# Kernel tuning notes

Measured on AMD Instinct MI355X. Metric: run time of the kernel, lower is better.

Reference implementation:

```python
import jax, jax.numpy as jnp
import numpy as np

B, S, D, H = 2, 4096, 512, 8
HD = D // H  # 64


def setup_inputs() -> dict:
    key = jax.random.key(0)
    ks = jax.random.split(key, 9)
    def lin_init(kw, kb, fan_in, fan_out):
        bound = 1.0 / np.sqrt(fan_in)
        W = jax.random.uniform(kw, (fan_in, fan_out), minval=-bound, maxval=bound, dtype=jnp.float32)
        b = jax.random.uniform(kb, (fan_out,), minval=-bound, maxval=bound, dtype=jnp.float32)
        return W, b
    Wq, bq = lin_init(ks[0], ks[1], D, D)
    Wk, bk = lin_init(ks[2], ks[3], D, D)
    Wv, bv = lin_init(ks[4], ks[5], D, D)
    query = jax.random.normal(ks[6], (B, S, D), dtype=jnp.float32)
    key_in = jax.random.normal(ks[7], (B, S, D), dtype=jnp.float32)
    value = jax.random.normal(ks[8], (B, S, D), dtype=jnp.float32)
    return {"query": query, "key": key_in, "value": value,
            "Wq": Wq, "bq": bq, "Wk": Wk, "bk": bk, "Wv": Wv, "bv": bv}


def _split_heads(x):
    # [B, S, D] -> [B, H, S, HD]
    b, s, _ = x.shape
    return x.reshape(b, s, H, HD).transpose(0, 2, 1, 3)


def reference(query, key, value, Wq, bq, Wk, bk, Wv, bv):
    Q = _split_heads(query @ Wq + bq)
    K = _split_heads(key @ Wk + bk)
    V = _split_heads(value @ Wv + bv)
    scale = 1.0 / np.sqrt(HD).astype(np.float32)
    # scores: [B, H, Sq, Sk]
    scores = jnp.einsum('bhqd,bhkd->bhqk', Q, K) * scale
    weights = jax.nn.softmax(scores, axis=-1)
    att = jnp.einsum('bhqk,bhkd->bhqd', weights, V)
    # [B, H, S, HD] -> [B, S, D]
    return att.transpose(0, 2, 1, 3).reshape(query.shape[0], query.shape[1], D)
```

## Files before the change

kernel.cpp:

```cpp
#include <hip/hip_runtime.h>
#include <hip/hip_bf16.h>
#include <cstdint>


typedef __bf16   bf16x8 __attribute__((ext_vector_type(8)));
typedef _Float16 f16x8  __attribute__((ext_vector_type(8)));
typedef float    f32x4  __attribute__((ext_vector_type(4)));
typedef float    f32x16 __attribute__((ext_vector_type(16)));
typedef unsigned int   u32;
typedef unsigned int   u32x4 __attribute__((ext_vector_type(4)));
typedef unsigned short u16;

#define NB  2
#define SEQ 4096
#define DIM 512
#define NH  8
#define HD  64
#define WSZ (DIM * DIM)
#define XSZ (NB * SEQ * DIM)
#define QSZ (NB * NH * SEQ * HD)

__device__ __forceinline__ u16 f2bf(float f) {
    __bf16 h = (__bf16)f; return __builtin_bit_cast(u16, h);
}
__device__ __forceinline__ u16 f2h(float f) {
    _Float16 h = (_Float16)f; return __builtin_bit_cast(u16, h);
}
__device__ __forceinline__ u32 pack_pkrtz(float a, float b) {
    auto pk = __builtin_amdgcn_cvt_pkrtz(a, b);
    return __builtin_bit_cast(u32, pk);
}
__device__ __forceinline__ bf16x8 cvt8p(float4 a, float4 b) {
    bf16x8 o;
    o[0]=(__bf16)a.x; o[1]=(__bf16)a.y; o[2]=(__bf16)a.z; o[3]=(__bf16)a.w;
    o[4]=(__bf16)b.x; o[5]=(__bf16)b.y; o[6]=(__bf16)b.z; o[7]=(__bf16)b.w;
    return o;
}
__device__ __forceinline__ void dma16(const u16* g, u16* l) {
    __builtin_amdgcn_global_load_lds(
        (const __attribute__((address_space(1))) u32*)g,
        (__attribute__((address_space(3))) u32*)l, 16, 0, 0);
}

__global__ __launch_bounds__(256) void xcvt_kernel(
    const float* __restrict__ xq, const float* __restrict__ xk,
    const float* __restrict__ xv, u16* __restrict__ xb)
{
    const int id = blockIdx.x;
    const int p = id >> 10, rest = id & 1023;
    const int mtile = rest >> 4, kk = rest & 15;
    const float* X = (p == 0) ? xq : ((p == 1) ? xk : xv);
    const int t = threadIdx.x;
    const int row = t >> 1, half = t & 1;
    const float* src = X + ((size_t)(mtile * 128 + row)) * DIM + kk * 32 + half * 16;
    u16* dst = xb + (size_t)p * XSZ + ((size_t)(mtile * 16 + kk)) * 4096 + row * 32;
    const int sr = (row ^ (row >> 2)) & 3;
    float4 a0 = ((const float4*)src)[0], a1 = ((const float4*)src)[1];
    float4 a2 = ((const float4*)src)[2], a3 = ((const float4*)src)[3];
    const int c0 = (half * 2) ^ sr, c1 = (half * 2 + 1) ^ sr;
    *(bf16x8*)(dst + (c0 << 3)) = cvt8p(a0, a1);
    *(bf16x8*)(dst + (c1 << 3)) = cvt8p(a2, a3);
}

__global__ __launch_bounds__(256) void wt_kernel(
    const float* __restrict__ Wq, const float* __restrict__ Wk,
    const float* __restrict__ Wv, u16* __restrict__ wtImg)
{
    __shared__ u16 lT[64 * 65];
    const int p = blockIdx.z;
    const float* W = (p == 0) ? Wq : ((p == 1) ? Wk : Wv);
    const int r0 = blockIdx.x * 64, c0 = blockIdx.y * 64;
    const int t = threadIdx.x;
#pragma unroll
    for (int i = 0; i < 16; i++) {
        int idx = i * 256 + t, rowk = idx >> 6, coln = idx & 63;
        lT[coln * 65 + rowk] = f2bf(W[(size_t)(r0 + rowk) * DIM + c0 + coln]);
    }
    __syncthreads();
#pragma unroll
    for (int i = 0; i < 2; i++) {
        const int idx = i * 256 + t;
        const int nl = idx >> 3, ch = idx & 7;
        const int n = c0 + nl;
        const int row = n & 127, ntile = n >> 7;
        const int kk = (r0 >> 5) + (ch >> 2);
        const int sw = (ch & 3) ^ ((row ^ (row >> 2)) & 3);
        u16* d = wtImg + (size_t)p * WSZ + ((size_t)(ntile * 16 + kk)) * 4096
               + row * 32 + (sw << 3);
#pragma unroll
        for (int e = 0; e < 8; e++) d[e] = lT[nl * 65 + ch * 8 + e];
    }
}

__global__ __launch_bounds__(256) void proj_kernel(
    const u16* __restrict__ xb, const u16* __restrict__ wtImg,
    const float* __restrict__ bq, const float* __restrict__ bk,
    const float* __restrict__ bv,
    u16* __restrict__ qb, u16* __restrict__ kbImg, u16* __restrict__ vtImg)
{
    __shared__ u16 smem[16384];

    const int tid = threadIdx.x;
    const int wave = tid >> 6, lane = tid & 63;
    const int l16 = lane & 15, quad = lane >> 4;
    const int wq = wave >> 1, wn = wave & 1;

    const int id = blockIdx.x;
    const int xcd = id & 7, j = id >> 3;
    const int p = j >> 5, t5 = j & 31;
    int mb, nb;
    if (p < 2) { mb = xcd * 8 + (t5 >> 2); nb = t5 & 3; }
    else       { nb = xcd * 8 + (t5 >> 2); mb = t5 & 3; }

    const u16* Abase = (p < 2) ? xb + (size_t)p * XSZ + (size_t)mb * 16 * 4096
                               : wtImg + (size_t)2 * WSZ + (size_t)mb * 16 * 4096;
    const u16* Bbase = (p < 2) ? wtImg + (size_t)p * WSZ + (size_t)nb * 16 * 4096
                               : xb + (size_t)2 * XSZ + (size_t)nb * 16 * 4096;
    const int doff = tid * 8;

    f32x4 acc[4][4];
#pragma unroll
    for (int ms = 0; ms < 4; ms++)
#pragma unroll
        for (int ns = 0; ns < 4; ns++)
#pragma unroll
            for (int jj = 0; jj < 4; jj++) acc[ms][ns][jj] = 0.f;

#pragma unroll
    for (int e = 0; e < 2; e++) {
        dma16(Abase + e * 2048 + doff, smem + e * 2048 + doff);
        dma16(Bbase + e * 2048 + doff, smem + 4096 + e * 2048 + doff);
    }
    Abase += 4096; Bbase += 4096;

    for (int kt = 0; kt < 16; kt++) {
        __syncthreads();
        if (kt < 15) {
            u16* lb = smem + ((kt + 1) & 1) * 8192;
#pragma unroll
            for (int e = 0; e < 2; e++) {
                dma16(Abase + e * 2048 + doff, lb + e * 2048 + doff);
                dma16(Bbase + e * 2048 + doff, lb + 4096 + e * 2048 + doff);
            }
            Abase += 4096; Bbase += 4096;
        }
        const u16* lA = smem + (kt & 1) * 8192;
        const u16* lB = lA + 4096;

        bf16x8 af[4];
#pragma unroll
        for (int ms = 0; ms < 4; ms++) {
            const int row = wq * 64 + ms * 16 + l16;
            const int sr = (row ^ (row >> 2)) & 3;
            af[ms] = *(const bf16x8*)&lA[row * 32 + ((quad ^ sr) << 3)];
        }
#pragma unroll
        for (int ns = 0; ns < 4; ns++) {
            const int rowb = wn * 64 + ns * 16 + l16;
            const int sb = (rowb ^ (rowb >> 2)) & 3;
            const bf16x8 b = *(const bf16x8*)&lB[rowb * 32 + ((quad ^ sb) << 3)];
#pragma unroll
            for (int ms = 0; ms < 4; ms++)
                acc[ms][ns] = __builtin_amdgcn_mfma_f32_16x16x32_bf16(af[ms], b, acc[ms][ns], 0, 0, 0);
        }
    }

    __syncthreads();
    if (p < 2) {
        const float* bias = p ? bk : bq;
        const float cs = (p == 0) ? 0.18033688011112042f : 1.0f;
        const int stl = wn * 2 + wq;
        const int hh = nb * 2 + wn;
#pragma unroll
        for (int ns = 0; ns < 4; ns++) {
            const int ch = ns * 16 + l16;
            const float bval = bias[hh * 64 + ch];
#pragma unroll
            for (int ms = 0; ms < 4; ms++)
#pragma unroll
                for (int rr = 0; rr < 4; rr++) {
                    const int sqL = ms * 16 + quad * 4 + rr;
                    const float v = (acc[ms][ns][rr] + bval) * cs;
                    int off;
                    if (p == 0) off = sqL * 64 + ch;
                    else        off = sqL * 64 +
                                      (((ch >> 3) ^ ((sqL ^ (sqL >> 3)) & 7)) << 3) + (ch & 7);
                    smem[stl * 4096 + off] = f2bf(v);
                }
        }
    } else {
        const int stl = wq * 2 + wn;
#pragma unroll
        for (int ms = 0; ms < 4; ms++)
#pragma unroll
            for (int rr = 0; rr < 4; rr++) {
                const int hd = ms * 16 + quad * 4 + rr;
                const float bval = bv[mb * 128 + wq * 64 + hd];
                const int swh = (hd ^ (hd >> 3)) & 7;
#pragma unroll
                for (int ns = 0; ns < 4; ns++) {
                    const int nl = ns * 16 + l16;
                    const int sqpL = (nl & ~12) | ((nl & 8) >> 1) | ((nl & 4) << 1);
                    smem[stl * 4096 + hd * 64 +
                         (((sqpL >> 3) ^ swh) << 3) + (sqpL & 7)] =
                        f2h(acc[ms][ns][rr] + bval);
                }
            }
    }
    __syncthreads();

    {
        u16* dstp; size_t gbase;
        if (p < 2) {
            const int hh = nb * 2 + (wave >> 1);
            const int b2 = mb >> 5;
            const int row0 = (mb * 128 + (wave & 1) * 64) & 4095;
            if (p == 0) { dstp = qb;    gbase = ((size_t)(b2 * NH + hh) * 4096 + row0) * 64; }
            else        { dstp = kbImg; gbase = ((size_t)((b2 * NH + hh) * 64 + (row0 >> 6))) * 4096; }
        } else {
            const int hh = mb * 2 + (wave >> 1);
            const int b2 = nb >> 5;
            const int nblk = (nb & 31) * 2 + (wave & 1);
            dstp = vtImg; gbase = ((size_t)((b2 * NH + hh) * 64 + nblk)) * 4096;
        }
#pragma unroll
        for (int e = 0; e < 8; e++) {
            const u32x4 vv = *(const u32x4*)&smem[wave * 4096 + e * 512 + lane * 8];
            *(u32x4*)(dstp + gbase + e * 512 + lane * 8) = vv;
        }
    }
}

__global__ __launch_bounds__(512, 4) void attn_kernel(
    const u16* __restrict__ qb, const u16* __restrict__ kbImg,
    const u16* __restrict__ vtImg, float* __restrict__ out)
{
    __shared__ u16 smem[2 * 4 * 4096];
    float* cmb = (float*)smem;

    const int tid = threadIdx.x;
    const int wave = tid >> 6, lane = tid & 63;
    const int m31 = lane & 31, h = lane >> 5;
    const int wq = wave >> 1, kh = wave & 1;

    const int blk = blockIdx.x;
    const int xcd = blk & 7, idx = blk >> 3;
    const int bh = xcd * 2 + (idx >> 5);
    const int qt = idx & 31;
    const int qbase = qt * 128 + wq * 32;

    bf16x8 qF[4];
#pragma unroll
    for (int c = 0; c < 4; c++)
        qF[c] = *(const bf16x8*)(qb + ((size_t)bh * SEQ + qbase + m31) * HD + c * 16 + h * 8);

    f32x16 O0, O1;
#pragma unroll
    for (int j = 0; j < 16; j++) { O0[j] = 0.f; O1[j] = 0.f; }
    float l_acc = 0.f;

    const int st  = wave >> 1;
    const int hw  = wave & 1;
    const u16* img = (st & 1) ? vtImg : kbImg;
    const u16* gp = img + ((size_t)(bh * 64 + (st >> 1) * 32)) * 4096 + hw * 2048 + lane * 8;
    {
        u16* lb = smem + st * 4096 + hw * 2048 + lane * 8;
#pragma unroll
        for (int e = 0; e < 4; e++) dma16(gp + e * 512, lb + e * 512);
        gp += 4096;
    }

    const int NT = 32;
    for (int it = 0; it < NT; it++) {
        __syncthreads();
        if (it + 1 < NT) {
            u16* lb = smem + ((((it + 1) & 1) * 4 + st)) * 4096 + hw * 2048 + lane * 8;
#pragma unroll
            for (int e = 0; e < 4; e++) dma16(gp + e * 512, lb + e * 512);
            gp += 4096;
        }
        const u16* sK = smem + (size_t)(((it & 1) * 4) + kh * 2) * 4096;
        const u16* sV = sK + 4096;

#pragma unroll
        for (int kg = 0; kg < 2; kg++) {
            const int rK = kg * 32 + m31;
            const int swK = (rK ^ (rK >> 3)) & 7;
            bf16x8 kA[4];
#pragma unroll
            for (int c = 0; c < 4; c++)
                kA[c] = *(const bf16x8*)&sK[(rK << 6) + (((2 * c + h) ^ swK) << 3)];

            const int swV0 = (m31 ^ (m31 >> 3)) & 7;
            const int rV1 = 32 + m31;
            const int swV1 = (rV1 ^ (rV1 >> 3)) & 7;
            f16x8 vA0[2], vA1[2];
#pragma unroll
            for (int c2 = 0; c2 < 2; c2++) {
                vA0[c2] = *(const f16x8*)&sV[(m31 << 6) + (((4 * kg + 2 * c2 + h) ^ swV0) << 3)];
                vA1[c2] = *(const f16x8*)&sV[(rV1 << 6) + (((4 * kg + 2 * c2 + h) ^ swV1) << 3)];
            }

            f32x16 Sv;
#pragma unroll
            for (int j = 0; j < 16; j++) Sv[j] = 0.f;
#pragma unroll
            for (int c = 0; c < 4; c++)
                Sv = __builtin_amdgcn_mfma_f32_32x32x16_bf16(kA[c], qF[c], Sv, 0, 0, 0);

            float ps = 0.f;
            u32 P32[8];
#pragma unroll
            for (int mm = 0; mm < 8; mm++) {
                const float e0 = __builtin_amdgcn_exp2f(Sv[2 * mm]);
                const float e1 = __builtin_amdgcn_exp2f(Sv[2 * mm + 1]);
                ps += e0 + e1;
                P32[mm] = pack_pkrtz(e0, e1);
            }
            l_acc += ps;

            u32x4 f0, f1;
            f0[0] = P32[0]; f0[1] = P32[1]; f0[2] = P32[2]; f0[3] = P32[3];
            f1[0] = P32[4]; f1[1] = P32[5]; f1[2] = P32[6]; f1[3] = P32[7];
            const f16x8 pf0 = __builtin_bit_cast(f16x8, f0);
            const f16x8 pf1 = __builtin_bit_cast(f16x8, f1);
            O0 = __builtin_amdgcn_mfma_f32_32x32x16_f16(vA0[0], pf0, O0, 0, 0, 0);
            O0 = __builtin_amdgcn_mfma_f32_32x32x16_f16(vA0[1], pf1, O0, 0, 0, 0);
            O1 = __builtin_amdgcn_mfma_f32_32x32x16_f16(vA1[0], pf0, O1, 0, 0, 0);
            O1 = __builtin_amdgcn_mfma_f32_32x32x16_f16(vA1[1], pf1, O1, 0, 0, 0);
        }
    }

    l_acc += __shfl_xor(l_acc, 32);
    __syncthreads();
    if (kh == 1) {
#pragma unroll
        for (int hg = 0; hg < 2; hg++)
#pragma unroll
            for (int mm = 0; mm < 4; mm++) {
                f32x4 o;
#pragma unroll
                for (int j = 0; j < 4; j++) o[j] = (hg ? O1 : O0)[4 * mm + j];
                *(f32x4*)&cmb[(((wq * 2 + hg) * 4 + mm) << 8) + lane * 4] = o;
            }
        cmb[8192 + wq * 64 + lane] = l_acc;
    }
    __syncthreads();

    if (kh == 0) {
        const int b = bh >> 3, hcol = bh & 7;
        const float lt = l_acc + cmb[8192 + wq * 64 + lane];
        const float inv = 1.0f / lt;
        const int sq = qbase + m31;
#pragma unroll
        for (int hg = 0; hg < 2; hg++)
#pragma unroll
            for (int mm = 0; mm < 4; mm++) {
                const f32x4 po = *(const f32x4*)&cmb[(((wq * 2 + hg) * 4 + mm) << 8) + lane * 4];
                f32x4 o;
#pragma unroll
                for (int j = 0; j < 4; j++)
                    o[j] = ((hg ? O1 : O0)[4 * mm + j] + po[j]) * inv;
                *(f32x4*)&out[(((size_t)(b * SEQ + sq)) << 9) + hcol * 64
                              + hg * 32 + 8 * mm + 4 * h] = o;
            }
    }
}

extern "C" void kernel_launch(void* const* d_in, const int* in_sizes, int n_in,
                              void* d_out, int out_size, void* d_ws, size_t ws_size,
                              hipStream_t stream)
{
    const float* q  = (const float*)d_in[0];
    const float* k  = (const float*)d_in[1];
    const float* v  = (const float*)d_in[2];
    const float* Wq = (const float*)d_in[3];
    const float* bq = (const float*)d_in[4];
    const float* Wk = (const float*)d_in[5];
    const float* bk = (const float*)d_in[6];
    const float* Wv = (const float*)d_in[7];
    const float* bv = (const float*)d_in[8];
    float* out = (float*)d_out;

    u16* xb  = (u16*)d_ws;
    u16* wti = xb  + (size_t)3 * XSZ;
    u16* qbp = wti + (size_t)3 * WSZ;
    u16* kbp = qbp + (size_t)QSZ;
    u16* vtp = kbp + (size_t)QSZ;

    xcvt_kernel<<<dim3(3072),   256, 0, stream>>>(q, k, v, xb);
    wt_kernel  <<<dim3(8, 8, 3), 256, 0, stream>>>(Wq, Wk, Wv, wti);
    proj_kernel<<<dim3(768),    256, 0, stream>>>(xb, wti, bq, bk, bv,
                                                  qbp, kbp, vtp);
    attn_kernel<<<dim3(512),    512, 0, stream>>>(qbp, kbp, vtp, out);
}
```

Before: 216.4 us.

## Fuse input bf16 conversion into projection and read K/V directly from global in attention

Drops the separate fp32-to-bf16 input conversion kernel. The projection kernel now loads fp32 activations into registers, converts them and writes swizzled bf16 into LDS, while weights are stored plainly transposed and DMA'd with the swizzle applied at load time. The attention kernel drops its LDS double-buffered K/V staging and reads K/V fragments straight from global memory (relying on cache), using smaller 256-thread blocks over 64-query tiles with twice as many blocks. This saves a kernel launch and a full intermediate write/read of the activations, but risks uncoalesced or cache-dependent global loads in attention and register pressure in the projection.

```diff
diff --git a/kernel.cpp b/kernel.cpp
--- a/kernel.cpp
+++ b/kernel.cpp
@@ -17,7 +17,6 @@
 #define NH  8
 #define HD  64
 #define WSZ (DIM * DIM)
-#define XSZ (NB * SEQ * DIM)
 #define QSZ (NB * NH * SEQ * HD)
 
 __device__ __forceinline__ u16 f2bf(float f) {
@@ -42,58 +41,32 @@
         (__attribute__((address_space(3))) u32*)l, 16, 0, 0);
 }
 
-__global__ __launch_bounds__(256) void xcvt_kernel(
-    const float* __restrict__ xq, const float* __restrict__ xk,
-    const float* __restrict__ xv, u16* __restrict__ xb)
-{
-    const int id = blockIdx.x;
-    const int p = id >> 10, rest = id & 1023;
-    const int mtile = rest >> 4, kk = rest & 15;
-    const float* X = (p == 0) ? xq : ((p == 1) ? xk : xv);
-    const int t = threadIdx.x;
-    const int row = t >> 1, half = t & 1;
-    const float* src = X + ((size_t)(mtile * 128 + row)) * DIM + kk * 32 + half * 16;
-    u16* dst = xb + (size_t)p * XSZ + ((size_t)(mtile * 16 + kk)) * 4096 + row * 32;
-    const int sr = (row ^ (row >> 2)) & 3;
-    float4 a0 = ((const float4*)src)[0], a1 = ((const float4*)src)[1];
-    float4 a2 = ((const float4*)src)[2], a3 = ((const float4*)src)[3];
-    const int c0 = (half * 2) ^ sr, c1 = (half * 2 + 1) ^ sr;
-    *(bf16x8*)(dst + (c0 << 3)) = cvt8p(a0, a1);
-    *(bf16x8*)(dst + (c1 << 3)) = cvt8p(a2, a3);
-}
-
 __global__ __launch_bounds__(256) void wt_kernel(
     const float* __restrict__ Wq, const float* __restrict__ Wk,
-    const float* __restrict__ Wv, u16* __restrict__ wtImg)
+    const float* __restrict__ Wv, u16* __restrict__ wt)
 {
     __shared__ u16 lT[64 * 65];
     const int p = blockIdx.z;
     const float* W = (p == 0) ? Wq : ((p == 1) ? Wk : Wv);
+    u16* dst = wt + (size_t)p * WSZ;
     const int r0 = blockIdx.x * 64, c0 = blockIdx.y * 64;
     const int t = threadIdx.x;
 #pragma unroll
     for (int i = 0; i < 16; i++) {
-        int idx = i * 256 + t, rowk = idx >> 6, coln = idx & 63;
-        lT[coln * 65 + rowk] = f2bf(W[(size_t)(r0 + rowk) * DIM + c0 + coln]);
+        int idx = i * 256 + t, row = idx >> 6, col = idx & 63;
+        lT[col * 65 + row] = f2bf(W[(size_t)(r0 + row) * DIM + c0 + col]);
     }
     __syncthreads();
 #pragma unroll
-    for (int i = 0; i < 2; i++) {
-        const int idx = i * 256 + t;
-        const int nl = idx >> 3, ch = idx & 7;
-        const int n = c0 + nl;
-        const int row = n & 127, ntile = n >> 7;
-        const int kk = (r0 >> 5) + (ch >> 2);
-        const int sw = (ch & 3) ^ ((row ^ (row >> 2)) & 3);
-        u16* d = wtImg + (size_t)p * WSZ + ((size_t)(ntile * 16 + kk)) * 4096
-               + row * 32 + (sw << 3);
-#pragma unroll
-        for (int e = 0; e < 8; e++) d[e] = lT[nl * 65 + ch * 8 + e];
+    for (int i = 0; i < 16; i++) {
+        int idx = i * 256 + t, n = idx >> 6, k = idx & 63;
+        dst[(size_t)(c0 + n) * DIM + r0 + k] = lT[n * 65 + k];
     }
 }
 
 __global__ __launch_bounds__(256) void proj_kernel(
-    const u16* __restrict__ xb, const u16* __restrict__ wtImg,
+    const float* __restrict__ xq, const float* __restrict__ xk,
+    const float* __restrict__ xv, const u16* __restrict__ wt,
     const float* __restrict__ bq, const float* __restrict__ bk,
     const float* __restrict__ bv,
     u16* __restrict__ qb, u16* __restrict__ kbImg, u16* __restrict__ vtImg)
@@ -112,11 +85,31 @@
     if (p < 2) { mb = xcd * 8 + (t5 >> 2); nb = t5 & 3; }
     else       { nb = xcd * 8 + (t5 >> 2); mb = t5 & 3; }
 
-    const u16* Abase = (p < 2) ? xb + (size_t)p * XSZ + (size_t)mb * 16 * 4096
-                               : wtImg + (size_t)2 * WSZ + (size_t)mb * 16 * 4096;
-    const u16* Bbase = (p < 2) ? wtImg + (size_t)p * WSZ + (size_t)nb * 16 * 4096
-                               : xb + (size_t)2 * XSZ + (size_t)nb * 16 * 4096;
-    const int doff = tid * 8;
+    const float* Xp = (p == 0) ? xq : ((p == 1) ? xk : xv);
+    const bool cvtA = (p < 2);
+    const int xtile = cvtA ? mb : nb;
+    const int wtile = cvtA ? nb : mb;
+    const float* Xbase = Xp + (size_t)xtile * 128 * DIM;
+    const u16*   Wbase = wt + (size_t)p * WSZ + (size_t)wtile * 128 * DIM;
+
+    u16* ldsX0 = smem + (cvtA ? 0 : 4096);
+    u16* ldsW0 = smem + (cvtA ? 4096 : 0);
+
+    const int xrow = tid >> 1, xhalf = tid & 1;
+    const int xsr = (xrow ^ (xrow >> 2)) & 3;
+    const float* xsrc = Xbase + (size_t)xrow * DIM + xhalf * 16;
+    const int xslot0 = xrow * 32 + (((xhalf * 2) ^ xsr) << 3);
+    const int xslot1 = xrow * 32 + (((xhalf * 2 + 1) ^ xsr) << 3);
+
+    int wslot[2]; const u16* wsrc[2];
+#pragma unroll
+    for (int e = 0; e < 2; e++) {
+        const int flat = e * 256 + tid;
+        const int row = flat >> 2, c = flat & 3;
+        const int gc = c ^ ((row ^ (row >> 2)) & 3);
+        wslot[e] = flat * 8;
+        wsrc[e]  = Wbase + (size_t)row * DIM + gc * 8;
+    }
 
     f32x4 acc[4][4];
 #pragma unroll
@@ -127,23 +120,30 @@
             for (int jj = 0; jj < 4; jj++) acc[ms][ns][jj] = 0.f;
 
 #pragma unroll
-    for (int e = 0; e < 2; e++) {
-        dma16(Abase + e * 2048 + doff, smem + e * 2048 + doff);
-        dma16(Bbase + e * 2048 + doff, smem + 4096 + e * 2048 + doff);
-    }
-    Abase += 4096; Bbase += 4096;
+    for (int e = 0; e < 2; e++) dma16(wsrc[e], ldsW0 + wslot[e]);
+    float4 rx0 = ((const float4*)xsrc)[0], rx1 = ((const float4*)xsrc)[1];
+    float4 rx2 = ((const float4*)xsrc)[2], rx3 = ((const float4*)xsrc)[3];
+    *(bf16x8*)(ldsX0 + xslot0) = cvt8p(rx0, rx1);
+    *(bf16x8*)(ldsX0 + xslot1) = cvt8p(rx2, rx3);
+    rx0 = ((const float4*)(xsrc + 32))[0]; rx1 = ((const float4*)(xsrc + 32))[1];
+    rx2 = ((const float4*)(xsrc + 32))[2]; rx3 = ((const float4*)(xsrc + 32))[3];
 
     for (int kt = 0; kt < 16; kt++) {
         __syncthreads();
+        const int nxt = (kt + 1) & 1;
         if (kt < 15) {
-            u16* lb = smem + ((kt + 1) & 1) * 8192;
-#pragma unroll
-            for (int e = 0; e < 2; e++) {
-                dma16(Abase + e * 2048 + doff, lb + e * 2048 + doff);
-                dma16(Bbase + e * 2048 + doff, lb + 4096 + e * 2048 + doff);
-            }
-            Abase += 4096; Bbase += 4096;
-        }
+#pragma unroll
+            for (int e = 0; e < 2; e++)
+                dma16(wsrc[e] + (kt + 1) * 32, ldsW0 + nxt * 8192 + wslot[e]);
+            *(bf16x8*)(ldsX0 + nxt * 8192 + xslot0) = cvt8p(rx0, rx1);
+            *(bf16x8*)(ldsX0 + nxt * 8192 + xslot1) = cvt8p(rx2, rx3);
+        }
+        if (kt < 14) {
+            const float* s = xsrc + (kt + 2) * 32;
+            rx0 = ((const float4*)s)[0]; rx1 = ((const float4*)s)[1];
+            rx2 = ((const float4*)s)[2]; rx3 = ((const float4*)s)[3];
+        }
+
         const u16* lA = smem + (kt & 1) * 8192;
         const u16* lB = lA + 4096;
 
@@ -231,12 +231,11 @@
     }
 }
 
-__global__ __launch_bounds__(512, 4) void attn_kernel(
+__global__ __launch_bounds__(256) void attn_kernel(
     const u16* __restrict__ qb, const u16* __restrict__ kbImg,
     const u16* __restrict__ vtImg, float* __restrict__ out)
 {
-    __shared__ u16 smem[2 * 4 * 4096];
-    float* cmb = (float*)smem;
+    __shared__ float cmb[4224];
 
     const int tid = threadIdx.x;
     const int wave = tid >> 6, lane = tid & 63;
@@ -245,60 +244,54 @@
 
     const int blk = blockIdx.x;
     const int xcd = blk & 7, idx = blk >> 3;
-    const int bh = xcd * 2 + (idx >> 5);
-    const int qt = idx & 31;
-    const int qbase = qt * 128 + wq * 32;
+    const int bh = xcd * 2 + (idx >> 6);
+    const int qt = idx & 63;
+    const int qbase = qt * 64 + wq * 32;
 
     bf16x8 qF[4];
 #pragma unroll
     for (int c = 0; c < 4; c++)
         qF[c] = *(const bf16x8*)(qb + ((size_t)bh * SEQ + qbase + m31) * HD + c * 16 + h * 8);
 
+    int koff[2][4], voff[2][2][2];
+#pragma unroll
+    for (int kg = 0; kg < 2; kg++) {
+        const int rK = kg * 32 + m31;
+        const int swK = (rK ^ (rK >> 3)) & 7;
+#pragma unroll
+        for (int c = 0; c < 4; c++)
+            koff[kg][c] = (rK << 6) + (((2 * c + h) ^ swK) << 3);
+#pragma unroll
+        for (int c2 = 0; c2 < 2; c2++)
+#pragma unroll
+            for (int rv = 0; rv < 2; rv++) {
+                const int row = rv * 32 + m31;
+                const int swV = (row ^ (row >> 3)) & 7;
+                voff[kg][c2][rv] = (row << 6) + (((4 * kg + 2 * c2 + h) ^ swV) << 3);
+            }
+    }
+
+    const u16* kbase = kbImg + (size_t)(bh * 64 + kh * 32) * 4096;
+    const u16* vbase = vtImg + (size_t)(bh * 64 + kh * 32) * 4096;
+
     f32x16 O0, O1;
 #pragma unroll
     for (int j = 0; j < 16; j++) { O0[j] = 0.f; O1[j] = 0.f; }
     float l_acc = 0.f;
 
-    const int st  = wave >> 1;
-    const int hw  = wave & 1;
-    const u16* img = (st & 1) ? vtImg : kbImg;
-    const u16* gp = img + ((size_t)(bh * 64 + (st >> 1) * 32)) * 4096 + hw * 2048 + lane * 8;
-    {
-        u16* lb = smem + st * 4096 + hw * 2048 + lane * 8;
-#pragma unroll
-        for (int e = 0; e < 4; e++) dma16(gp + e * 512, lb + e * 512);
-        gp += 4096;
-    }
-
-    const int NT = 32;
-    for (int it = 0; it < NT; it++) {
-        __syncthreads();
-        if (it + 1 < NT) {
-            u16* lb = smem + ((((it + 1) & 1) * 4 + st)) * 4096 + hw * 2048 + lane * 8;
-#pragma unroll
-            for (int e = 0; e < 4; e++) dma16(gp + e * 512, lb + e * 512);
-            gp += 4096;
-        }
-        const u16* sK = smem + (size_t)(((it & 1) * 4) + kh * 2) * 4096;
-        const u16* sV = sK + 4096;
-
+#pragma unroll 2
+    for (int it = 0; it < 32; it++) {
 #pragma unroll
         for (int kg = 0; kg < 2; kg++) {
-            const int rK = kg * 32 + m31;
-            const int swK = (rK ^ (rK >> 3)) & 7;
             bf16x8 kA[4];
 #pragma unroll
             for (int c = 0; c < 4; c++)
-                kA[c] = *(const bf16x8*)&sK[(rK << 6) + (((2 * c + h) ^ swK) << 3)];
-
-            const int swV0 = (m31 ^ (m31 >> 3)) & 7;
-            const int rV1 = 32 + m31;
-            const int swV1 = (rV1 ^ (rV1 >> 3)) & 7;
+                kA[c] = *(const bf16x8*)(kbase + koff[kg][c]);
             f16x8 vA0[2], vA1[2];
 #pragma unroll
             for (int c2 = 0; c2 < 2; c2++) {
-                vA0[c2] = *(const f16x8*)&sV[(m31 << 6) + (((4 * kg + 2 * c2 + h) ^ swV0) << 3)];
-                vA1[c2] = *(const f16x8*)&sV[(rV1 << 6) + (((4 * kg + 2 * c2 + h) ^ swV1) << 3)];
+                vA0[c2] = *(const f16x8*)(vbase + voff[kg][c2][0]);
+                vA1[c2] = *(const f16x8*)(vbase + voff[kg][c2][1]);
             }
 
             f32x16 Sv;
@@ -329,10 +322,11 @@
             O1 = __builtin_amdgcn_mfma_f32_32x32x16_f16(vA1[0], pf0, O1, 0, 0, 0);
             O1 = __builtin_amdgcn_mfma_f32_32x32x16_f16(vA1[1], pf1, O1, 0, 0, 0);
         }
+        kbase += 4096;
+        vbase += 4096;
     }
 
     l_acc += __shfl_xor(l_acc, 32);
-    __syncthreads();
     if (kh == 1) {
 #pragma unroll
         for (int hg = 0; hg < 2; hg++)
@@ -343,13 +337,13 @@
                 for (int j = 0; j < 4; j++) o[j] = (hg ? O1 : O0)[4 * mm + j];
                 *(f32x4*)&cmb[(((wq * 2 + hg) * 4 + mm) << 8) + lane * 4] = o;
             }
-        cmb[8192 + wq * 64 + lane] = l_acc;
+        cmb[4096 + wq * 64 + lane] = l_acc;
     }
     __syncthreads();
 
     if (kh == 0) {
         const int b = bh >> 3, hcol = bh & 7;
-        const float lt = l_acc + cmb[8192 + wq * 64 + lane];
+        const float lt = l_acc + cmb[4096 + wq * 64 + lane];
         const float inv = 1.0f / lt;
         const int sq = qbase + m31;
 #pragma unroll
@@ -382,15 +376,13 @@
     const float* bv = (const float*)d_in[8];
     float* out = (float*)d_out;
 
-    u16* xb  = (u16*)d_ws;
-    u16* wti = xb  + (size_t)3 * XSZ;
-    u16* qbp = wti + (size_t)3 * WSZ;
+    u16* wt  = (u16*)d_ws;
+    u16* qbp = wt  + (size_t)3 * WSZ;
     u16* kbp = qbp + (size_t)QSZ;
     u16* vtp = kbp + (size_t)QSZ;
 
-    xcvt_kernel<<<dim3(3072),   256, 0, stream>>>(q, k, v, xb);
-    wt_kernel  <<<dim3(8, 8, 3), 256, 0, stream>>>(Wq, Wk, Wv, wti);
-    proj_kernel<<<dim3(768),    256, 0, stream>>>(xb, wti, bq, bk, bv,
-                                                  qbp, kbp, vtp);
-    attn_kernel<<<dim3(512),    512, 0, stream>>>(qbp, kbp, vtp, out);
-}
+    wt_kernel  <<<dim3(8, 8, 3), 256, 0, stream>>>(Wq, Wk, Wv, wt);
+    proj_kernel<<<dim3(768),     256, 0, stream>>>(q, k, v, wt, bq, bk, bv,
+                                                   qbp, kbp, vtp);
+    attn_kernel<<<dim3(1024),    256, 0, stream>>>(qbp, kbp, vtp, out);
+}
```

Measured after the change: 267.7 us. +23.7%, slower.
